# Optimization experiments

Measured on AMD Instinct MI355X. Metric: run time of the kernel, lower is better.

## Reference

```python
import jax, jax.numpy as jnp
import numpy as np

D = 1024      # model dim
H = 16        # num heads
HD = D // H   # head dim = 64
B, N, M = 4, 4096, 256
EPS = 1e-12   # torch F.normalize eps


def setup_inputs() -> dict:
    key = jax.random.key(0)
    ks = jax.random.split(key, 11)
    s = 0.02  # weight init scale
    W = lambda k: jax.random.normal(k, (D, D), jnp.float32) * s
    return {
        "x": jax.random.normal(ks[0], (B, N, D), jnp.float32),
        "c": jax.random.normal(ks[1], (B, M, D), jnp.float32),
        "Wq_x": W(ks[2]), "Wk_x": W(ks[3]), "Wv_x": W(ks[4]),
        "Wq_c": W(ks[5]), "Wk_c": W(ks[6]), "Wv_c": W(ks[7]),
        "Wo_x": W(ks[8]), "Wo_c": W(ks[9]),
        "norm_const": 0.5 * jnp.ones((1, H, 1, 1), jnp.float32),
    }


def _heads(t):
    # (B, S, D) -> (B, H, S, HD)
    b, s, _ = t.shape
    return t.reshape(b, s, H, HD).transpose(0, 2, 1, 3)


def _l2norm(t):
    n = jnp.linalg.norm(t, axis=-1, keepdims=True)
    return t / jnp.maximum(n, EPS)


def reference(x, c, Wq_x, Wk_x, Wv_x, Wq_c, Wk_c, Wv_c, Wo_x, Wo_c, norm_const):
    b, n, d = x.shape
    m = c.shape[1]
    # fused QKV projections for each stream (Linear, no bias: y = t @ W^T)
    qx = _l2norm(_heads(x @ Wq_x.T))   # (B,H,N,HD), cosine-normalized
    kx = _l2norm(_heads(x @ Wk_x.T))
    vx = _heads(x @ Wv_x.T)
    qc = _l2norm(_heads(c @ Wq_c.T))   # (B,H,M,HD)
    kc = _l2norm(_heads(c @ Wk_c.T))
    vc = _heads(c @ Wv_c.T)
    # concat streams along the sequence axis
    q = jnp.concatenate([qx, qc], axis=2)   # (B,H,N+M,HD)
    k = jnp.concatenate([kx, kc], axis=2)
    v = jnp.concatenate([vx, vc], axis=2)
    n_tot = n + m
    # cosine (linear) attention, non-causal: values scaled by N^sigmoid(norm_const)
    v = v / (jnp.float32(n_tot) ** jax.nn.sigmoid(norm_const))
    kv = jnp.einsum("bhnd,bhne->bhde", k, v)         # (B,H,HD,HD)
    attn = jnp.einsum("bhnd,bhde->bhne", q, kv)      # (B,H,N+M,HD)
    # split streams, merge heads, output projections
    attn_x = attn[:, :, :n].transpose(0, 2, 1, 3).reshape(b, n, H * HD)
    attn_c = attn[:, :, n:].transpose(0, 2, 1, 3).reshape(b, m, H * HD)
    out_x = attn_x @ Wo_x.T
    out_c = attn_c @ Wo_c.T
    return out_x, out_c
```

## Files before the change

kernel.cpp:

```cpp
#include <hip/hip_runtime.h>
#include <cstdint>

typedef unsigned int u32;
typedef unsigned short u16;
typedef float fx4 __attribute__((ext_vector_type(4)));
typedef __bf16 bfx8 __attribute__((ext_vector_type(8)));

__device__ __forceinline__ u16 f2bf(float f) {
  u32 u = __builtin_bit_cast(u32, f);
  u32 r = (u + 0x7fffu + ((u >> 16) & 1u)) >> 16;
  return (u16)r;
}
__device__ __forceinline__ float bf2f(u16 v) {
  return __builtin_bit_cast(float, (u32)v << 16);
}
__device__ __forceinline__ void async_copy16(const void* g, void* l) {
  auto gp = reinterpret_cast<__attribute__((address_space(1))) void*>((uintptr_t)g);
  auto lp = reinterpret_cast<__attribute__((address_space(3))) void*>((uintptr_t)l);
  __builtin_amdgcn_global_load_lds(gp, lp, 16, 0, 0);
}

__global__ __launch_bounds__(256) void cvt_all(
    const float* __restrict__ x, const float* __restrict__ c,
    const float* __restrict__ w0, const float* __restrict__ w1,
    const float* __restrict__ w2, const float* __restrict__ w3,
    const float* __restrict__ w4, const float* __restrict__ w5,
    const float* __restrict__ w6, const float* __restrict__ w7,
    u16* __restrict__ xb, u16* __restrict__ cb, u16* __restrict__ wb) {
  const int i = blockIdx.x * 256 + threadIdx.x;
  const float* src;
  u16* dst;
  size_t off;
  if (i < 4194304) {
    src = x; dst = xb; off = (size_t)i;
  } else if (i < 4456448) {
    src = c; dst = cb; off = (size_t)(i - 4194304);
  } else {
    const int r = i - 4456448;
    const int wsel = r >> 18;
    off = (size_t)(r & 262143);
    switch (wsel) {
      case 0: src = w0; break; case 1: src = w1; break;
      case 2: src = w2; break; case 3: src = w3; break;
      case 4: src = w4; break; case 5: src = w5; break;
      case 6: src = w6; break; default: src = w7; break;
    }
    dst = wb + (size_t)wsel * 1048576;
  }
  const fx4 v = *(const fx4*)(src + off * 4);
  uint2 o;
  o.x = (u32)f2bf(v[0]) | ((u32)f2bf(v[1]) << 16);
  o.y = (u32)f2bf(v[2]) | ((u32)f2bf(v[3]) << 16);
  *(uint2*)(dst + off * 4) = o;
}

__device__ __forceinline__ void gemm_core_k1024(
    const u16* __restrict__ A, const u16* __restrict__ Bw,
    long rowBase, long colBase, u16* As, u16* Bs, fx4 (&acc)[4][4]) {
  const int t = threadIdx.x;
  const int lane = t & 63;
  const int lr = lane & 15;
  const int quad = lane >> 4;
  const int sw = lr & 7;
  const int w = t >> 6;
  const int m0 = (w & 1) * 64;
  const int n0 = (w >> 1) * 64;
  const int f0 = t * 8;

  for (int k0 = 0; k0 < 1024; k0 += 64) {
#pragma unroll
    for (int r = 0; r < 4; ++r) {
      const int f = f0 + r * 2048;
      const int row = f >> 6;
      const int gst = (f >> 3) & 7;
      const int col = ((gst ^ (row & 7)) << 3);
      async_copy16(A + (rowBase + row) * 1024 + (k0 + col), &As[f]);
      async_copy16(Bw + (colBase + row) * 1024 + (k0 + col), &Bs[f]);
    }
    __syncthreads();
#pragma unroll
    for (int ks = 0; ks < 2; ++ks) {
      bfx8 af[4], bfr[4];
      const int g = ((ks * 4 + quad) ^ sw) << 3;
#pragma unroll
      for (int i = 0; i < 4; ++i)
        af[i] = *(const bfx8*)&As[(m0 + i * 16 + lr) * 64 + g];
#pragma unroll
      for (int i = 0; i < 4; ++i)
        bfr[i] = *(const bfx8*)&Bs[(n0 + i * 16 + lr) * 64 + g];
#pragma unroll
      for (int mi = 0; mi < 4; ++mi)
#pragma unroll
        for (int ni = 0; ni < 4; ++ni)
          acc[mi][ni] =
              __builtin_amdgcn_mfma_f32_16x16x32_bf16(af[mi], bfr[ni], acc[mi][ni], 0, 0, 0);
    }
    __syncthreads();
  }
}

__global__ __launch_bounds__(256) void proj_fused(
    const u16* __restrict__ Xb, const u16* __restrict__ Cb, const u16* __restrict__ Wb,
    u16* __restrict__ Qx, u16* __restrict__ Kx, u16* __restrict__ Vx,
    u16* __restrict__ Qc, u16* __restrict__ Kc, u16* __restrict__ Vc,
    const float* __restrict__ nc) {
  __shared__ __align__(16) u16 As[128 * 64];
  __shared__ __align__(16) u16 Bs[128 * 64];
  const bool isC = blockIdx.y >= 128;
  const u16* A = isC ? Cb : Xb;
  const u16* Bw = Wb + (isC ? 3145728 : 0);
  const long rowBase = (long)(isC ? blockIdx.y - 128 : blockIdx.y) * 128;
  const long colBase = (long)blockIdx.x * 128;

  fx4 acc[4][4] = {};
  gemm_core_k1024(A, Bw, rowBase, colBase, As, Bs, acc);

  const int t = threadIdx.x;
  const int lane = t & 63;
  const int lr = lane & 15;
  const int quad = lane >> 4;
  const int w = t >> 6;
  const int m0 = (w & 1) * 64;
  const int n0 = (w >> 1) * 64;

  const long col0 = colBase + n0;
  const int col64 = (int)(col0 >> 6);
  const int sel = col64 >> 4;
  const int h = col64 & 15;
  const int lcolBase = (int)(col0 & 1023);
  u16* dst;
  if (sel == 0) dst = isC ? Qc : Qx;
  else if (sel == 1) dst = isC ? Kc : Kx;
  else dst = isC ? Vc : Vx;

  if (sel < 2) {
#pragma unroll
    for (int mi = 0; mi < 4; ++mi) {
      float ss[4] = {0.f, 0.f, 0.f, 0.f};
#pragma unroll
      for (int ni = 0; ni < 4; ++ni)
#pragma unroll
        for (int r = 0; r < 4; ++r) ss[r] += acc[mi][ni][r] * acc[mi][ni][r];
#pragma unroll
      for (int off = 1; off < 16; off <<= 1)
#pragma unroll
        for (int r = 0; r < 4; ++r) ss[r] += __shfl_xor(ss[r], off, 64);
      float sc[4];
#pragma unroll
      for (int r = 0; r < 4; ++r) sc[r] = 1.f / fmaxf(sqrtf(ss[r]), 1e-12f);
#pragma unroll
      for (int ni = 0; ni < 4; ++ni) {
        const long col = lcolBase + ni * 16 + lr;
#pragma unroll
        for (int r = 0; r < 4; ++r) {
          const long row = rowBase + m0 + mi * 16 + quad * 4 + r;
          dst[row * 1024 + col] = f2bf(acc[mi][ni][r] * sc[r]);
        }
      }
    }
  } else {
    const float s = __expf(-8.3783908f / (1.f + __expf(-nc[h])));
#pragma unroll
    for (int mi = 0; mi < 4; ++mi)
#pragma unroll
      for (int ni = 0; ni < 4; ++ni) {
        const long col = lcolBase + ni * 16 + lr;
#pragma unroll
        for (int r = 0; r < 4; ++r) {
          const long row = rowBase + m0 + mi * 16 + quad * 4 + r;
          dst[row * 1024 + col] = f2bf(acc[mi][ni][r] * s);
        }
      }
  }
}

__global__ __launch_bounds__(256) void out_fused(
    const u16* __restrict__ Qx, const u16* __restrict__ Qc,
    const u16* __restrict__ Wex, const u16* __restrict__ Wec,
    float* __restrict__ out) {
  __shared__ __align__(16) u16 As[128 * 64];
  __shared__ __align__(16) u16 Bs[128 * 64];
  const int yt = blockIdx.y;
  const int b = yt / 34;
  const int local = yt - b * 34;
  const bool isC = local >= 32;
  const u16* A;
  const u16* Bw;
  float* C;
  long rowBase;
  if (!isC) {
    A = Qx + (size_t)b * 4194304;
    Bw = Wex + (size_t)b * 1048576;
    C = out + (size_t)b * 4194304;
    rowBase = (long)local * 128;
  } else {
    A = Qc + (size_t)b * 262144;
    Bw = Wec + (size_t)b * 1048576;
    C = out + 16777216 + (size_t)b * 262144;
    rowBase = (long)(local - 32) * 128;
  }
  const long colBase = (long)blockIdx.x * 128;

  fx4 acc[4][4] = {};
  gemm_core_k1024(A, Bw, rowBase, colBase, As, Bs, acc);

  const int t = threadIdx.x;
  const int lane = t & 63;
  const int lr = lane & 15;
  const int quad = lane >> 4;
  const int w = t >> 6;
  const int m0 = (w & 1) * 64;
  const int n0 = (w >> 1) * 64;
#pragma unroll
  for (int mi = 0; mi < 4; ++mi)
#pragma unroll
    for (int ni = 0; ni < 4; ++ni) {
      const long col = colBase + n0 + ni * 16 + lr;
#pragma unroll
      for (int r = 0; r < 4; ++r) {
        const long row = rowBase + m0 + mi * 16 + quad * 4 + r;
        C[row * 1024 + col] = acc[mi][ni][r];
      }
    }
}

__global__ __launch_bounds__(256) void kv_partial(
    const u16* __restrict__ Kx, const u16* __restrict__ Vx,
    const u16* __restrict__ Kc, const u16* __restrict__ Vc,
    float* __restrict__ part) {
  const int split = blockIdx.x;
  const int bh = blockIdx.y;
  const int b = bh >> 4, h = bh & 15;
  const u16* Kp;
  const u16* Vp;
  size_t rowBase;
  if (split < 16) { Kp = Kx; Vp = Vx; rowBase = (size_t)b * 4096 + (size_t)split * 256; }
  else           { Kp = Kc; Vp = Vc; rowBase = (size_t)b * 256; }

  __shared__ __align__(16) float Ks[64 * 64];
  __shared__ __align__(16) float Vs[64 * 64];
  const int t = threadIdx.x;
  const int db = (t >> 4) * 4;
  const int eb = (t & 15) * 4;
  float acc[4][4] = {};

  for (int ch = 0; ch < 4; ++ch) {
#pragma unroll
    for (int j = 0; j < 2; ++j) {
      const int u = t + 256 * j;
      const int row = u >> 3, grp = u & 7;
      const size_t goff = (rowBase + ch * 64 + row) * 1024 + h * 64 + grp * 8;
      const uint4 kq = *(const uint4*)(Kp + goff);
      const uint4 vq = *(const uint4*)(Vp + goff);
      float* kd = &Ks[row * 64 + grp * 8];
      float* vd = &Vs[row * 64 + grp * 8];
      kd[0] = bf2f((u16)(kq.x & 0xffff)); kd[1] = bf2f((u16)(kq.x >> 16));
      kd[2] = bf2f((u16)(kq.y & 0xffff)); kd[3] = bf2f((u16)(kq.y >> 16));
      kd[4] = bf2f((u16)(kq.z & 0xffff)); kd[5] = bf2f((u16)(kq.z >> 16));
      kd[6] = bf2f((u16)(kq.w & 0xffff)); kd[7] = bf2f((u16)(kq.w >> 16));
      vd[0] = bf2f((u16)(vq.x & 0xffff)); vd[1] = bf2f((u16)(vq.x >> 16));
      vd[2] = bf2f((u16)(vq.y & 0xffff)); vd[3] = bf2f((u16)(vq.y >> 16));
      vd[4] = bf2f((u16)(vq.z & 0xffff)); vd[5] = bf2f((u16)(vq.z >> 16));
      vd[6] = bf2f((u16)(vq.w & 0xffff)); vd[7] = bf2f((u16)(vq.w >> 16));
    }
    __syncthreads();
#pragma unroll 4
    for (int n = 0; n < 64; ++n) {
      const fx4 kd = *(const fx4*)&Ks[n * 64 + db];
      const fx4 ve = *(const fx4*)&Vs[n * 64 + eb];
#pragma unroll
      for (int i = 0; i < 4; ++i)
#pragma unroll
        for (int j = 0; j < 4; ++j)
          acc[i][j] += kd[i] * ve[j];
    }
    __syncthreads();
  }
  float* pp = part + ((size_t)bh * 17 + split) * 4096;
#pragma unroll
  for (int i = 0; i < 4; ++i)
#pragma unroll
    for (int j = 0; j < 4; ++j)
      pp[(db + i) * 64 + (eb + j)] = acc[i][j];
}

__global__ __launch_bounds__(256) void kv_reduce(const float* __restrict__ part,
                                                 float* __restrict__ kv) {
  const int i = blockIdx.x * 256 + threadIdx.x;
  const int bh = i >> 12;
  const int de = i & 4095;
  float s = 0.f;
#pragma unroll
  for (int sp = 0; sp < 17; ++sp) s += part[((size_t)bh * 17 + sp) * 4096 + de];
  kv[i] = s;
}

__global__ __launch_bounds__(256) void weff_build(
    const u16* __restrict__ WoX, const u16* __restrict__ WoC,
    const float* __restrict__ kvb, u16* __restrict__ WeffX, u16* __restrict__ WeffC) {
  const int ot = blockIdx.x;
  const int bh = blockIdx.y;
  const int b = bh >> 4, h = bh & 15;
  const u16* Wo = blockIdx.z ? WoC : WoX;
  u16* outp = (blockIdx.z ? WeffC : WeffX) + (size_t)b * 1048576;

  __shared__ __align__(16) float kvT[64 * 64];
  __shared__ __align__(16) float WoT[64 * 64];
  const int t = threadIdx.x;
#pragma unroll
  for (int j = 0; j < 4; ++j) {
    const int idx = (t + 256 * j) * 4;
    const fx4 v = *(const fx4*)&kvb[(size_t)bh * 4096 + idx];
    const int d = idx >> 6;
    const int e0 = idx & 63;
#pragma unroll
    for (int k = 0; k < 4; ++k) kvT[(e0 + k) * 64 + d] = v[k];
  }
#pragma unroll
  for (int j = 0; j < 2; ++j) {
    const int u = t + 256 * j;
    const int row = u >> 3;
    const int e0 = (u & 7) * 8;
    const uint4 q = *(const uint4*)&Wo[(size_t)(ot * 64 + row) * 1024 + h * 64 + e0];
    WoT[(e0 + 0) * 64 + row] = bf2f((u16)(q.x & 0xffff));
    WoT[(e0 + 1) * 64 + row] = bf2f((u16)(q.x >> 16));
    WoT[(e0 + 2) * 64 + row] = bf2f((u16)(q.y & 0xffff));
    WoT[(e0 + 3) * 64 + row] = bf2f((u16)(q.y >> 16));
    WoT[(e0 + 4) * 64 + row] = bf2f((u16)(q.z & 0xffff));
    WoT[(e0 + 5) * 64 + row] = bf2f((u16)(q.z >> 16));
    WoT[(e0 + 6) * 64 + row] = bf2f((u16)(q.w & 0xffff));
    WoT[(e0 + 7) * 64 + row] = bf2f((u16)(q.w >> 16));
  }
  __syncthreads();
  const int ob = (t >> 4) * 4;
  const int db = (t & 15) * 4;
  float acc[4][4] = {};
#pragma unroll 4
  for (int e = 0; e < 64; ++e) {
    const fx4 wv = *(const fx4*)&WoT[e * 64 + ob];
    const fx4 kvv = *(const fx4*)&kvT[e * 64 + db];
#pragma unroll
    for (int i = 0; i < 4; ++i)
#pragma unroll
      for (int j = 0; j < 4; ++j)
        acc[i][j] += wv[i] * kvv[j];
  }
#pragma unroll
  for (int i = 0; i < 4; ++i)
#pragma unroll
    for (int j = 0; j < 4; ++j)
      outp[(size_t)(ot * 64 + ob + i) * 1024 + h * 64 + db + j] = f2bf(acc[i][j]);
}

extern "C" void kernel_launch(void* const* d_in, const int* in_sizes, int n_in,
                              void* d_out, int out_size, void* d_ws, size_t ws_size,
                              hipStream_t stream) {
  (void)in_sizes; (void)n_in; (void)out_size; (void)ws_size;
  const float* x = (const float*)d_in[0];
  const float* c = (const float*)d_in[1];
  const float* nc = (const float*)d_in[10];
  float* out = (float*)d_out;
  char* ws = (char*)d_ws;

  u16* Xb = (u16*)(ws + 0);
  u16* Cb = (u16*)(ws + 33554432);
  u16* Wb = (u16*)(ws + 35651584);
  u16* Qx = (u16*)(ws + 52428800);
  u16* Kx = (u16*)(ws + 85983232);
  u16* Vx = (u16*)(ws + 119537664);
  u16* Qc = (u16*)(ws + 153092096);
  u16* Kc = (u16*)(ws + 155189248);
  u16* Vc = (u16*)(ws + 157286400);
  float* part = (float*)(ws + 159383552);
  float* kvb = (float*)(ws + 177209344);
  u16* Weffx = (u16*)(ws + 178257920);
  u16* Weffc = (u16*)(ws + 186646528);

  cvt_all<<<25600, 256, 0, stream>>>(
      x, c, (const float*)d_in[2], (const float*)d_in[3], (const float*)d_in[4],
      (const float*)d_in[5], (const float*)d_in[6], (const float*)d_in[7],
      (const float*)d_in[8], (const float*)d_in[9], Xb, Cb, Wb);

  proj_fused<<<dim3(24, 136), 256, 0, stream>>>(Xb, Cb, Wb, Qx, Kx, Vx, Qc, Kc, Vc, nc);
  kv_partial<<<dim3(17, 64), 256, 0, stream>>>(Kx, Vx, Kc, Vc, part);
  kv_reduce<<<1024, 256, 0, stream>>>(part, kvb);
  weff_build<<<dim3(16, 64, 2), 256, 0, stream>>>(Wb + 6 * 1048576, Wb + 7 * 1048576,
                                                  kvb, Weffx, Weffc);
  out_fused<<<dim3(8, 136), 256, 0, stream>>>(Qx, Qc, Weffx, Weffc, out);
}
```

Baseline: 439.4 us.

## Store K/V transposed per head and compute KV with MFMA in one kernel

The projection epilogue now writes K and V transposed into a per-(batch,head) [64 x 4352] layout. It goes through a swizzled LDS staging buffer, and the x and c streams are concatenated along the sequence axis. A new kv_mfma kernel replaces the scalar-FMA kv_partial plus kv_reduce pair. It computes K^T V with bf16 MFMA using async global-to-LDS copies and reduces the four waves' partials in LDS, which removes the partial-sum buffer round trip. The trade-off is that only 64 blocks run the KV stage, which risks underusing the GPU, and the projection epilogue gains an extra LDS transpose and barrier.

```diff
diff --git a/kernel.cpp b/kernel.cpp
--- a/kernel.cpp
+++ b/kernel.cpp
@@ -101,11 +101,12 @@
 
 __global__ __launch_bounds__(256) void proj_fused(
     const u16* __restrict__ Xb, const u16* __restrict__ Cb, const u16* __restrict__ Wb,
-    u16* __restrict__ Qx, u16* __restrict__ Kx, u16* __restrict__ Vx,
-    u16* __restrict__ Qc, u16* __restrict__ Kc, u16* __restrict__ Vc,
+    u16* __restrict__ Qx, u16* __restrict__ Qc,
+    u16* __restrict__ Kt, u16* __restrict__ Vt,
     const float* __restrict__ nc) {
-  __shared__ __align__(16) u16 As[128 * 64];
-  __shared__ __align__(16) u16 Bs[128 * 64];
+  __shared__ __align__(16) u16 LDSbuf[2 * 128 * 64];
+  u16* As = LDSbuf;
+  u16* Bs = LDSbuf + 8192;
   const bool isC = blockIdx.y >= 128;
   const u16* A = isC ? Cb : Xb;
   const u16* Bw = Wb + (isC ? 3145728 : 0);
@@ -128,12 +129,9 @@
   const int sel = col64 >> 4;
   const int h = col64 & 15;
   const int lcolBase = (int)(col0 & 1023);
-  u16* dst;
-  if (sel == 0) dst = isC ? Qc : Qx;
-  else if (sel == 1) dst = isC ? Kc : Kx;
-  else dst = isC ? Vc : Vx;
-
-  if (sel < 2) {
+
+  if (sel == 0) {
+    u16* dst = isC ? Qc : Qx;
 #pragma unroll
     for (int mi = 0; mi < 4; ++mi) {
       float ss[4] = {0.f, 0.f, 0.f, 0.f};
@@ -159,19 +157,176 @@
       }
     }
   } else {
-    const float s = __expf(-8.3783908f / (1.f + __expf(-nc[h])));
-#pragma unroll
-    for (int mi = 0; mi < 4; ++mi)
+    u16* LT = LDSbuf + w * 4096;
+    u16* T = (sel == 1) ? Kt : Vt;
+    const long R0 = rowBase + m0;
+    int b, nglob0;
+    if (!isC) { b = (int)(R0 >> 12); nglob0 = (int)(R0 & 4095); }
+    else      { b = (int)(R0 >> 8);  nglob0 = 4096 + (int)(R0 & 255); }
+    u16* Tw = T + (size_t)(b * 16 + h) * 64 * 4352;
+    const float vs = __expf(-8.3783908f / (1.f + __expf(-nc[h])));
+
+#pragma unroll
+    for (int mi = 0; mi < 4; ++mi) {
+      float sc[4];
+      if (sel == 1) {
+        float ss[4] = {0.f, 0.f, 0.f, 0.f};
+#pragma unroll
+        for (int ni = 0; ni < 4; ++ni)
+#pragma unroll
+          for (int r = 0; r < 4; ++r) ss[r] += acc[mi][ni][r] * acc[mi][ni][r];
+#pragma unroll
+        for (int off = 1; off < 16; off <<= 1)
+#pragma unroll
+          for (int r = 0; r < 4; ++r) ss[r] += __shfl_xor(ss[r], off, 64);
+#pragma unroll
+        for (int r = 0; r < 4; ++r) sc[r] = 1.f / fmaxf(sqrtf(ss[r]), 1e-12f);
+      } else {
+#pragma unroll
+        for (int r = 0; r < 4; ++r) sc[r] = vs;
+      }
+      const int g = 2 * mi + (quad >> 1);
+      const int sub = (quad & 1) * 4;
 #pragma unroll
       for (int ni = 0; ni < 4; ++ni) {
-        const long col = lcolBase + ni * 16 + lr;
-#pragma unroll
-        for (int r = 0; r < 4; ++r) {
-          const long row = rowBase + m0 + mi * 16 + quad * 4 + r;
-          dst[row * 1024 + col] = f2bf(acc[mi][ni][r] * s);
-        }
+        const int d = ni * 16 + lr;
+        uint2 o;
+        o.x = (u32)f2bf(acc[mi][ni][0] * sc[0]) | ((u32)f2bf(acc[mi][ni][1] * sc[1]) << 16);
+        o.y = (u32)f2bf(acc[mi][ni][2] * sc[2]) | ((u32)f2bf(acc[mi][ni][3] * sc[3]) << 16);
+        *(uint2*)&LT[d * 64 + ((g ^ (d & 7)) << 3) + sub] = o;
       }
-  }
+    }
+    __syncthreads();
+    const int d = lane;
+    u16* drow = Tw + (size_t)d * 4352 + nglob0;
+#pragma unroll
+    for (int j = 0; j < 8; ++j) {
+      const uint4 qv = *(const uint4*)&LT[d * 64 + ((j ^ (d & 7)) << 3)];
+      *(uint4*)&drow[j * 8] = qv;
+    }
+  }
+}
+
+__global__ __launch_bounds__(256) void kv_mfma(
+    const u16* __restrict__ Kt, const u16* __restrict__ Vt, float* __restrict__ kvb) {
+  __shared__ __align__(16) u16 TT[4][2][4096];
+  const int bh = blockIdx.x;
+  const int t = threadIdx.x;
+  const int w = t >> 6;
+  const int lane = t & 63;
+  const int lr = lane & 15;
+  const int quad = lane >> 4;
+  const u16* Ksrc = Kt + (size_t)bh * 64 * 4352;
+  const u16* Vsrc = Vt + (size_t)bh * 64 * 4352;
+  const int row8 = lane >> 3;
+  const int gst = lane & 7;
+  fx4 acc[4][4] = {};
+
+  for (int s = 0; s < 17; ++s) {
+    const int kbase = w * 1088 + s * 64;
+#pragma unroll
+    for (int i = 0; i < 8; ++i) {
+      const int row = i * 8 + row8;
+      const int col = ((gst ^ (row & 7)) << 3);
+      const size_t go = (size_t)row * 4352 + kbase + col;
+      async_copy16(Ksrc + go, &TT[w][0][i * 512 + lane * 8]);
+      async_copy16(Vsrc + go, &TT[w][1][i * 512 + lane * 8]);
+    }
+    __syncthreads();
+#pragma unroll
+    for (int ks = 0; ks < 2; ++ks) {
+      bfx8 af[4], bfr[4];
+      const int g = ((ks * 4 + quad) ^ (lr & 7)) << 3;
+#pragma unroll
+      for (int i = 0; i < 4; ++i) af[i] = *(const bfx8*)&TT[w][0][(i * 16 + lr) * 64 + g];
+#pragma unroll
+      for (int i = 0; i < 4; ++i) bfr[i] = *(const bfx8*)&TT[w][1][(i * 16 + lr) * 64 + g];
+#pragma unroll
+      for (int mi = 0; mi < 4; ++mi)
+#pragma unroll
+        for (int ni = 0; ni < 4; ++ni)
+          acc[mi][ni] =
+              __builtin_amdgcn_mfma_f32_16x16x32_bf16(af[mi], bfr[ni], acc[mi][ni], 0, 0, 0);
+    }
+    __syncthreads();
+  }
+  float* red = (float*)&TT[0][0][0];
+  float* my = red + w * 4096;
+#pragma unroll
+  for (int mi = 0; mi < 4; ++mi)
+#pragma unroll
+    for (int ni = 0; ni < 4; ++ni) {
+      const int e = ni * 16 + lr;
+      const int dg = mi * 4 + quad;
+      *(fx4*)&my[e * 64 + ((dg ^ (e & 15)) << 2)] = acc[mi][ni];
+    }
+  __syncthreads();
+  float* outp = kvb + (size_t)bh * 4096;
+#pragma unroll
+  for (int j = 0; j < 4; ++j) {
+    const int L = t * 16 + j * 4;
+    const int e = L >> 6;
+    const int dg = (L >> 2) & 15;
+    const int addr = e * 64 + ((dg ^ (e & 15)) << 2);
+    fx4 sv = *(const fx4*)&red[addr];
+    sv += *(const fx4*)&red[4096 + addr];
+    sv += *(const fx4*)&red[8192 + addr];
+    sv += *(const fx4*)&red[12288 + addr];
+    *(fx4*)&outp[L] = sv;
+  }
+}
+
+__global__ __launch_bounds__(256) void weff_build(
+    const u16* __restrict__ WoX, const u16* __restrict__ WoC,
+    const float* __restrict__ kvb, u16* __restrict__ WeffX, u16* __restrict__ WeffC) {
+  const int ot = blockIdx.x;
+  const int bh = blockIdx.y;
+  const int b = bh >> 4, h = bh & 15;
+  const u16* Wo = blockIdx.z ? WoC : WoX;
+  u16* outp = (blockIdx.z ? WeffC : WeffX) + (size_t)b * 1048576;
+
+  __shared__ __align__(16) float kvT[64 * 64];
+  __shared__ __align__(16) float WoT[64 * 64];
+  const int t = threadIdx.x;
+#pragma unroll
+  for (int j = 0; j < 4; ++j) {
+    const int idx = (t + 256 * j) * 4;
+    *(fx4*)&kvT[idx] = *(const fx4*)&kvb[(size_t)bh * 4096 + idx];
+  }
+#pragma unroll
+  for (int j = 0; j < 2; ++j) {
+    const int u = t + 256 * j;
+    const int row = u >> 3;
+    const int e0 = (u & 7) * 8;
+    const uint4 q = *(const uint4*)&Wo[(size_t)(ot * 64 + row) * 1024 + h * 64 + e0];
+    WoT[(e0 + 0) * 64 + row] = bf2f((u16)(q.x & 0xffff));
+    WoT[(e0 + 1) * 64 + row] = bf2f((u16)(q.x >> 16));
+    WoT[(e0 + 2) * 64 + row] = bf2f((u16)(q.y & 0xffff));
+    WoT[(e0 + 3) * 64 + row] = bf2f((u16)(q.y >> 16));
+    WoT[(e0 + 4) * 64 + row] = bf2f((u16)(q.z & 0xffff));
+    WoT[(e0 + 5) * 64 + row] = bf2f((u16)(q.z >> 16));
+    WoT[(e0 + 6) * 64 + row] = bf2f((u16)(q.w & 0xffff));
+    WoT[(e0 + 7) * 64 + row] = bf2f((u16)(q.w >> 16));
+  }
+  __syncthreads();
+  const int ob = (t >> 4) * 4;
+  const int db = (t & 15) * 4;
+  float acc[4][4] = {};
+#pragma unroll 4
+  for (int e = 0; e < 64; ++e) {
+    const fx4 wv = *(const fx4*)&WoT[e * 64 + ob];
+    const fx4 kvv = *(const fx4*)&kvT[e * 64 + db];
+#pragma unroll
+    for (int i = 0; i < 4; ++i)
+#pragma unroll
+      for (int j = 0; j < 4; ++j)
+        acc[i][j] += wv[i] * kvv[j];
+  }
+#pragma unroll
+  for (int i = 0; i < 4; ++i)
+#pragma unroll
+    for (int j = 0; j < 4; ++j)
+      outp[(size_t)(ot * 64 + ob + i) * 1024 + h * 64 + db + j] = f2bf(acc[i][j]);
 }
 
 __global__ __launch_bounds__(256) void out_fused(
@@ -224,134 +379,6 @@
     }
 }
 
-__global__ __launch_bounds__(256) void kv_partial(
-    const u16* __restrict__ Kx, const u16* __restrict__ Vx,
-    const u16* __restrict__ Kc, const u16* __restrict__ Vc,
-    float* __restrict__ part) {
-  const int split = blockIdx.x;
-  const int bh = blockIdx.y;
-  const int b = bh >> 4, h = bh & 15;
-  const u16* Kp;
-  const u16* Vp;
-  size_t rowBase;
-  if (split < 16) { Kp = Kx; Vp = Vx; rowBase = (size_t)b * 4096 + (size_t)split * 256; }
-  else           { Kp = Kc; Vp = Vc; rowBase = (size_t)b * 256; }
-
-  __shared__ __align__(16) float Ks[64 * 64];
-  __shared__ __align__(16) float Vs[64 * 64];
-  const int t = threadIdx.x;
-  const int db = (t >> 4) * 4;
-  const int eb = (t & 15) * 4;
-  float acc[4][4] = {};
-
-  for (int ch = 0; ch < 4; ++ch) {
-#pragma unroll
-    for (int j = 0; j < 2; ++j) {
-      const int u = t + 256 * j;
-      const int row = u >> 3, grp = u & 7;
-      const size_t goff = (rowBase + ch * 64 + row) * 1024 + h * 64 + grp * 8;
-      const uint4 kq = *(const uint4*)(Kp + goff);
-      const uint4 vq = *(const uint4*)(Vp + goff);
-      float* kd = &Ks[row * 64 + grp * 8];
-      float* vd = &Vs[row * 64 + grp * 8];
-      kd[0] = bf2f((u16)(kq.x & 0xffff)); kd[1] = bf2f((u16)(kq.x >> 16));
-      kd[2] = bf2f((u16)(kq.y & 0xffff)); kd[3] = bf2f((u16)(kq.y >> 16));
-      kd[4] = bf2f((u16)(kq.z & 0xffff)); kd[5] = bf2f((u16)(kq.z >> 16));
-      kd[6] = bf2f((u16)(kq.w & 0xffff)); kd[7] = bf2f((u16)(kq.w >> 16));
-      vd[0] = bf2f((u16)(vq.x & 0xffff)); vd[1] = bf2f((u16)(vq.x >> 16));
-      vd[2] = bf2f((u16)(vq.y & 0xffff)); vd[3] = bf2f((u16)(vq.y >> 16));
-      vd[4] = bf2f((u16)(vq.z & 0xffff)); vd[5] = bf2f((u16)(vq.z >> 16));
-      vd[6] = bf2f((u16)(vq.w & 0xffff)); vd[7] = bf2f((u16)(vq.w >> 16));
-    }
-    __syncthreads();
-#pragma unroll 4
-    for (int n = 0; n < 64; ++n) {
-      const fx4 kd = *(const fx4*)&Ks[n * 64 + db];
-      const fx4 ve = *(const fx4*)&Vs[n * 64 + eb];
-#pragma unroll
-      for (int i = 0; i < 4; ++i)
-#pragma unroll
-        for (int j = 0; j < 4; ++j)
-          acc[i][j] += kd[i] * ve[j];
-    }
-    __syncthreads();
-  }
-  float* pp = part + ((size_t)bh * 17 + split) * 4096;
-#pragma unroll
-  for (int i = 0; i < 4; ++i)
-#pragma unroll
-    for (int j = 0; j < 4; ++j)
-      pp[(db + i) * 64 + (eb + j)] = acc[i][j];
-}
-
-__global__ __launch_bounds__(256) void kv_reduce(const float* __restrict__ part,
-                                                 float* __restrict__ kv) {
-  const int i = blockIdx.x * 256 + threadIdx.x;
-  const int bh = i >> 12;
-  const int de = i & 4095;
-  float s = 0.f;
-#pragma unroll
-  for (int sp = 0; sp < 17; ++sp) s += part[((size_t)bh * 17 + sp) * 4096 + de];
-  kv[i] = s;
-}
-
-__global__ __launch_bounds__(256) void weff_build(
-    const u16* __restrict__ WoX, const u16* __restrict__ WoC,
-    const float* __restrict__ kvb, u16* __restrict__ WeffX, u16* __restrict__ WeffC) {
-  const int ot = blockIdx.x;
-  const int bh = blockIdx.y;
-  const int b = bh >> 4, h = bh & 15;
-  const u16* Wo = blockIdx.z ? WoC : WoX;
-  u16* outp = (blockIdx.z ? WeffC : WeffX) + (size_t)b * 1048576;
-
-  __shared__ __align__(16) float kvT[64 * 64];
-  __shared__ __align__(16) float WoT[64 * 64];
-  const int t = threadIdx.x;
-#pragma unroll
-  for (int j = 0; j < 4; ++j) {
-    const int idx = (t + 256 * j) * 4;
-    const fx4 v = *(const fx4*)&kvb[(size_t)bh * 4096 + idx];
-    const int d = idx >> 6;
-    const int e0 = idx & 63;
-#pragma unroll
-    for (int k = 0; k < 4; ++k) kvT[(e0 + k) * 64 + d] = v[k];
-  }
-#pragma unroll
-  for (int j = 0; j < 2; ++j) {
-    const int u = t + 256 * j;
-    const int row = u >> 3;
-    const int e0 = (u & 7) * 8;
-    const uint4 q = *(const uint4*)&Wo[(size_t)(ot * 64 + row) * 1024 + h * 64 + e0];
-    WoT[(e0 + 0) * 64 + row] = bf2f((u16)(q.x & 0xffff));
-    WoT[(e0 + 1) * 64 + row] = bf2f((u16)(q.x >> 16));
-    WoT[(e0 + 2) * 64 + row] = bf2f((u16)(q.y & 0xffff));
-    WoT[(e0 + 3) * 64 + row] = bf2f((u16)(q.y >> 16));
-    WoT[(e0 + 4) * 64 + row] = bf2f((u16)(q.z & 0xffff));
-    WoT[(e0 + 5) * 64 + row] = bf2f((u16)(q.z >> 16));
-    WoT[(e0 + 6) * 64 + row] = bf2f((u16)(q.w & 0xffff));
-    WoT[(e0 + 7) * 64 + row] = bf2f((u16)(q.w >> 16));
-  }
-  __syncthreads();
-  const int ob = (t >> 4) * 4;
-  const int db = (t & 15) * 4;
-  float acc[4][4] = {};
-#pragma unroll 4
-  for (int e = 0; e < 64; ++e) {
-    const fx4 wv = *(const fx4*)&WoT[e * 64 + ob];
-    const fx4 kvv = *(const fx4*)&kvT[e * 64 + db];
-#pragma unroll
-    for (int i = 0; i < 4; ++i)
-#pragma unroll
-      for (int j = 0; j < 4; ++j)
-        acc[i][j] += wv[i] * kvv[j];
-  }
-#pragma unroll
-  for (int i = 0; i < 4; ++i)
-#pragma unroll
-    for (int j = 0; j < 4; ++j)
-      outp[(size_t)(ot * 64 + ob + i) * 1024 + h * 64 + db + j] = f2bf(acc[i][j]);
-}
-
 extern "C" void kernel_launch(void* const* d_in, const int* in_sizes, int n_in,
                               void* d_out, int out_size, void* d_ws, size_t ws_size,
                               hipStream_t stream) {
@@ -366,24 +393,20 @@
   u16* Cb = (u16*)(ws + 33554432);
   u16* Wb = (u16*)(ws + 35651584);
   u16* Qx = (u16*)(ws + 52428800);
-  u16* Kx = (u16*)(ws + 85983232);
-  u16* Vx = (u16*)(ws + 119537664);
-  u16* Qc = (u16*)(ws + 153092096);
-  u16* Kc = (u16*)(ws + 155189248);
-  u16* Vc = (u16*)(ws + 157286400);
-  float* part = (float*)(ws + 159383552);
-  float* kvb = (float*)(ws + 177209344);
-  u16* Weffx = (u16*)(ws + 178257920);
-  u16* Weffc = (u16*)(ws + 186646528);
+  u16* Qc = (u16*)(ws + 85983232);
+  u16* Kt = (u16*)(ws + 88080384);
+  u16* Vt = (u16*)(ws + 123731968);
+  float* kvb = (float*)(ws + 159383552);
+  u16* Weffx = (u16*)(ws + 160432128);
+  u16* Weffc = (u16*)(ws + 168820736);
 
   cvt_all<<<25600, 256, 0, stream>>>(
       x, c, (const float*)d_in[2], (const float*)d_in[3], (const float*)d_in[4],
       (const float*)d_in[5], (const float*)d_in[6], (const float*)d_in[7],
       (const float*)d_in[8], (const float*)d_in[9], Xb, Cb, Wb);
 
-  proj_fused<<<dim3(24, 136), 256, 0, stream>>>(Xb, Cb, Wb, Qx, Kx, Vx, Qc, Kc, Vc, nc);
-  kv_partial<<<dim3(17, 64), 256, 0, stream>>>(Kx, Vx, Kc, Vc, part);
-  kv_reduce<<<1024, 256, 0, stream>>>(part, kvb);
+  proj_fused<<<dim3(24, 136), 256, 0, stream>>>(Xb, Cb, Wb, Qx, Qc, Kt, Vt, nc);
+  kv_mfma<<<64, 256, 0, stream>>>(Kt, Vt, kvb);
   weff_build<<<dim3(16, 64, 2), 256, 0, stream>>>(Wb + 6 * 1048576, Wb + 7 * 1048576,
                                                   kvb, Weffx, Weffc);
   out_fused<<<dim3(8, 136), 256, 0, stream>>>(Qx, Qc, Weffx, Weffc, out);
```

Measured after the change: 428.1 us. 1.03x faster.
